# Performance work log

Hardware: AMD Instinct MI355X
Metric: run time of the kernel (lower is better)

## Reference

```python
import jax, jax.numpy as jnp
import numpy as np

B, T, S, D, H, HD, DFF, NB = 2, 2048, 2048, 768, 12, 64, 3072, 32
HID = H * HD
EPS = 1e-6
NEG = -1e9


def rmsnorm(x, w):
    # T5 RMSNorm: no mean subtraction, no bias
    var = jnp.mean(jnp.square(x), axis=-1, keepdims=True)
    return x * jax.lax.rsqrt(var + EPS) * w


def sdpa(h, kv, m, wq, wk, wv, wo):
    # h: [B,Tq,D], kv: [B,Tk,D], m: additive mask broadcastable to [B,H,Tq,Tk]
    b, tq, _ = h.shape
    tk = kv.shape[1]
    q = (h @ wq).reshape(b, tq, H, HD)
    k = (kv @ wk).reshape(b, tk, H, HD)
    v = (kv @ wv).reshape(b, tk, H, HD)
    scores = jnp.einsum('bthd,bshd->bhts', q, k) + m  # scale=1.0 (T5)
    p = jax.nn.softmax(scores, axis=-1)
    y = jnp.einsum('bhts,bshd->bthd', p, v).reshape(b, tq, HID)
    return y @ wo


def setup_inputs() -> dict:
    key = jax.random.key(0)
    ks = jax.random.split(key, 16)
    x = jax.random.normal(ks[0], (B, T, D), dtype=jnp.float32)
    # causal additive mask for decoder self-attention
    causal = jnp.tril(jnp.ones((T, T), dtype=bool))
    mask = jnp.broadcast_to(jnp.where(causal, 0.0, NEG)[None, None], (B, 1, T, T)).astype(jnp.float32)
    relative_position = jax.random.randint(ks[1], (1, 1, T, T), 0, NB)
    encoder_hidden_states = jax.random.normal(ks[2], (B, S, D), dtype=jnp.float32)
    encoder_attention_mask = jnp.zeros((B, 1, T, S), dtype=jnp.float32)
    sc = 0.02
    p = {
        'sn_w': jnp.ones((D,), jnp.float32),
        'wq': sc * jax.random.normal(ks[3], (D, HID)),
        'wk': sc * jax.random.normal(ks[4], (D, HID)),
        'wv': sc * jax.random.normal(ks[5], (D, HID)),
        'wo': sc * jax.random.normal(ks[6], (HID, D)),
        'rel_emb': sc * jax.random.normal(ks[7], (NB, H)),
        'cn_w': jnp.ones((D,), jnp.float32),
        'cwq': sc * jax.random.normal(ks[8], (D, HID)),
        'cwk': sc * jax.random.normal(ks[9], (D, HID)),
        'cwv': sc * jax.random.normal(ks[10], (D, HID)),
        'cwo': sc * jax.random.normal(ks[11], (HID, D)),
        'pn_w': jnp.ones((D,), jnp.float32),
        'ffn_wi': sc * jax.random.normal(ks[12], (D, DFF)),
        'ffn_wo': sc * jax.random.normal(ks[13], (DFF, D)),
    }
    return dict(x=x, mask=mask, relative_position=relative_position,
                encoder_hidden_states=encoder_hidden_states,
                encoder_attention_mask=encoder_attention_mask, **p)


def reference(x, mask, relative_position, encoder_hidden_states, encoder_attention_mask,
              sn_w, wq, wk, wv, wo, rel_emb, cn_w, cwq, cwk, cwv, cwo, pn_w, ffn_wi, ffn_wo):
    # self-attention with relative-position bias added into additive mask
    h = rmsnorm(x, sn_w)
    # rel_emb[relative_position]: [1,1,T,T,H] -> permute(0,1,4,2,3) -> squeeze(0) -> [1,H,T,T]
    position_bias = jnp.transpose(rel_emb[relative_position], (0, 1, 4, 2, 3))[0]
    self_mask = mask + position_bias
    y = sdpa(h, h, self_mask, wq, wk, wv, wo)
    attn_out = y + x
    # cross-attention (no relative bias -> zeros position bias)
    enc_dec_position_bias = jnp.zeros_like(encoder_attention_mask)
    h2 = rmsnorm(attn_out, cn_w)
    y2 = sdpa(h2, encoder_hidden_states, encoder_attention_mask + enc_dec_position_bias,
              cwq, cwk, cwv, cwo)
    attn_out = y2 + attn_out
    # T5 FFN: relu(x @ wi) @ wo, pre-norm, residual
    hn = rmsnorm(attn_out, pn_w)
    ff = jax.nn.relu(hn @ ffn_wi) @ ffn_wo
    return (attn_out + ff, position_bias, enc_dec_position_bias)
```

## Files before the change

kernel.cpp:

```cpp
#include <hip/hip_runtime.h>
#include <hip/hip_bf16.h>
#include <stdint.h>

#define T5_B   2
#define T5_T   2048
#define T5_S   2048
#define T5_D   768
#define T5_H   12
#define T5_HD  64
#define T5_DFF 3072
#define T5_NB  32
#define NROW   4096

typedef __attribute__((ext_vector_type(8))) short bf16x8;
typedef __attribute__((ext_vector_type(4))) short short4v;
typedef __attribute__((ext_vector_type(4))) float f32x4;

__device__ __forceinline__ unsigned short f2bf(float x) {
  unsigned int u = __float_as_uint(x);
  unsigned int r = (u + 0x7FFFu + ((u >> 16) & 1u)) >> 16;
  return (unsigned short)r;
}

__device__ __forceinline__ void load_lds16(const void* g, void* l) {
  __builtin_amdgcn_global_load_lds(
      (__attribute__((address_space(1))) void*)(const_cast<void*>(g)),
      (__attribute__((address_space(3))) void*)(l), 16, 0, 0);
}

__device__ __forceinline__ unsigned cvt_pk_bf16(float lo_, float hi_) {
  unsigned d;
  asm("v_cvt_pk_bf16_f32 %0, %1, %2" : "=v"(d) : "v"(lo_), "v"(hi_));
  return d;
}

__device__ __forceinline__ f32x4 mfma16(short4v a, short4v b, f32x4 c) {
#if __has_builtin(__builtin_amdgcn_mfma_f32_16x16x16bf16_1k)
  return __builtin_amdgcn_mfma_f32_16x16x16bf16_1k(a, b, c, 0, 0, 0);
#else
  asm volatile("v_mfma_f32_16x16x16_bf16 %0, %1, %2, %0" : "+v"(c) : "v"(a), "v"(b));
  return c;
#endif
}

struct PrepArgs {
  const float* wsrc[10];
  unsigned short* wdst[10];
  const float* enc; unsigned short* encb;
  const int* rp; unsigned char* rp8;
};

__global__ __launch_bounds__(256)
void prep_kernel(PrepArgs a) {
  __shared__ float tile[32][33];
  const int bid = blockIdx.x, tid = threadIdx.x;
  if (bid < 9216) {
    int widx, rem, Kd, Nd;
    if (bid < 4608)      { widx = bid / 576; rem = bid % 576;  Kd = 768;  Nd = 768;  }
    else if (bid < 6912) { widx = 8;         rem = bid - 4608; Kd = 768;  Nd = 3072; }
    else                 { widx = 9;         rem = bid - 6912; Kd = 3072; Nd = 768;  }
    const float* W = a.wsrc[widx];
    unsigned short* Wt = a.wdst[widx];
    int nb = Nd / 32;
    int n0 = (rem % nb) * 32, k0 = (rem / nb) * 32;
    int tx = tid & 31, ty = tid >> 5;
#pragma unroll
    for (int i = 0; i < 32; i += 8)
      tile[ty + i][tx] = W[(size_t)(k0 + ty + i) * Nd + n0 + tx];
    __syncthreads();
#pragma unroll
    for (int i = 0; i < 32; i += 8)
      Wt[(size_t)(n0 + ty + i) * Kd + k0 + tx] = f2bf(tile[tx][ty + i]);
  } else if (bid < 12288) {
    int i = (bid - 9216) * 256 + tid;
    float4 v = ((const float4*)a.enc)[i];
    unsigned long long pk = (unsigned long long)f2bf(v.x)
                          | ((unsigned long long)f2bf(v.y) << 16)
                          | ((unsigned long long)f2bf(v.z) << 32)
                          | ((unsigned long long)f2bf(v.w) << 48);
    *(unsigned long long*)(a.encb + (size_t)i * 4) = pk;
  } else {
    int idx = (bid - 12288) * 256 + tid;
    const int4* src = (const int4*)(a.rp + (size_t)idx * 16);
    int4 v0 = src[0], v1 = src[1], v2 = src[2], v3 = src[3];
    uint4 o;
    o.x = (v0.x & 31) | ((v0.y & 31) << 8) | ((v0.z & 31) << 16) | ((v0.w & 31) << 24);
    o.y = (v1.x & 31) | ((v1.y & 31) << 8) | ((v1.z & 31) << 16) | ((v1.w & 31) << 24);
    o.z = (v2.x & 31) | ((v2.y & 31) << 8) | ((v2.z & 31) << 16) | ((v2.w & 31) << 24);
    o.w = (v3.x & 31) | ((v3.y & 31) << 8) | ((v3.z & 31) << 16) | ((v3.w & 31) << 24);
    ((uint4*)a.rp8)[idx] = o;
  }
}

__global__ __launch_bounds__(256)
void rmsnorm_kernel(const float* __restrict__ in, const float* __restrict__ w,
                    unsigned short* __restrict__ out) {
  int row = blockIdx.x, tid = threadIdx.x;
  const float* r = in + (size_t)row * 768;
  float x0 = r[tid], x1 = r[tid + 256], x2 = r[tid + 512];
  float s = x0 * x0 + x1 * x1 + x2 * x2;
#pragma unroll
  for (int off = 32; off > 0; off >>= 1) s += __shfl_xor(s, off);
  __shared__ float ws_[4];
  int lane = tid & 63, wv = tid >> 6;
  if (lane == 0) ws_[wv] = s;
  __syncthreads();
  float tot = ws_[0] + ws_[1] + ws_[2] + ws_[3];
  float rinv = rsqrtf(tot * (1.0f / 768.0f) + 1e-6f);
  unsigned short* o = out + (size_t)row * 768;
  o[tid]       = f2bf(x0 * rinv * w[tid]);
  o[tid + 256] = f2bf(x1 * rinv * w[tid + 256]);
  o[tid + 512] = f2bf(x2 * rinv * w[tid + 512]);
}

__global__ __launch_bounds__(256)
void pos_bias_kernel(const int* __restrict__ rp, const float* __restrict__ rel_emb,
                     float* __restrict__ out1) {
  __shared__ float rl[384];
  int tid = threadIdx.x;
  for (int i = tid; i < 384; i += 256) rl[i] = rel_emb[i];
  __syncthreads();
  int t = blockIdx.y;
  int s = blockIdx.x * 1024 + tid * 4;
  int4 nb = *(const int4*)(rp + (size_t)t * 2048 + s);
#pragma unroll
  for (int h = 0; h < 12; ++h) {
    float4 v = make_float4(rl[nb.x * 12 + h], rl[nb.y * 12 + h],
                           rl[nb.z * 12 + h], rl[nb.w * 12 + h]);
    *(float4*)(out1 + ((size_t)h * 2048 + t) * 2048 + s) = v;
  }
}

__global__ __launch_bounds__(256)
void transpose_v_kernel(const unsigned short* __restrict__ vin, int stride,
                        unsigned short* __restrict__ vT) {
  __shared__ __align__(16) unsigned short tile[64][72];
  int t0 = blockIdx.x * 64, h = blockIdx.y, b = blockIdx.z;
  int tid = threadIdx.x;
  {
    int tl = tid >> 2, d0 = (tid & 3) * 16;
    const unsigned short* src = vin + (size_t)(b * 2048 + t0 + tl) * stride + h * 64 + d0;
    *(bf16x8*)&tile[tl][d0]     = *(const bf16x8*)src;
    *(bf16x8*)&tile[tl][d0 + 8] = *(const bf16x8*)(src + 8);
  }
  __syncthreads();
  {
    int d = tid >> 2, t1 = (tid & 3) * 16;
    unsigned short tmp[16] __attribute__((aligned(16)));
#pragma unroll
    for (int j = 0; j < 16; ++j) tmp[j] = tile[t1 + j][d];
    unsigned short* dst = vT + ((size_t)((b * 12 + h) * 64 + d)) * 2048 + t0 + t1;
    *(bf16x8*)dst       = *(bf16x8*)&tmp[0];
    *(bf16x8*)(dst + 8) = *(bf16x8*)&tmp[8];
  }
}

template <int TM, int TN, int EPI>
__global__ __launch_bounds__(256)
void gemm_bt(const unsigned short* __restrict__ A, const unsigned short* __restrict__ Bt,
             void* __restrict__ C, const float* __restrict__ res, int N, int K) {
  constexpr int WR = (TM >= 128) ? 2 : 1;
  constexpr int WC = 4 / WR;
  constexpr int AM = TM / WR / 16;
  constexpr int AN = TN / WC / 16;
  constexpr int CHA = TM / 8, CHB = TN / 8, CPW = (CHA + CHB) / 4;
  __shared__ __align__(16) unsigned short Als[TM * 64];
  __shared__ __align__(16) unsigned short Bls[TN * 64];
  const int tid = threadIdx.x, lane = tid & 63, wv = tid >> 6;
  const int lo = lane & 15, hi = lane >> 4;
  const int wr = wv / WC, wc = wv % WC;
  const int m0 = blockIdx.y * TM, n0 = blockIdx.x * TN;

  f32x4 acc[AM][AN];
#pragma unroll
  for (int i = 0; i < AM; ++i)
#pragma unroll
    for (int j = 0; j < AN; ++j) acc[i][j] = f32x4{0.f, 0.f, 0.f, 0.f};

  const int srr  = lane >> 3;
  const int scol = ((lane & 7) ^ srr) * 8;

  for (int k0 = 0; k0 < K; k0 += 64) {
    __syncthreads();
#pragma unroll
    for (int j = 0; j < CPW; ++j) {
      int c = wv * CPW + j;
      if (c < CHA)
        load_lds16(A + (size_t)(m0 + c * 8 + srr) * K + k0 + scol, Als + c * 512);
      else {
        int c2 = c - CHA;
        load_lds16(Bt + (size_t)(n0 + c2 * 8 + srr) * K + k0 + scol, Bls + c2 * 512);
      }
    }
    __syncthreads();
#pragma unroll
    for (int kk = 0; kk < 2; ++kk) {
      bf16x8 af[AM], bfr[AN];
#pragma unroll
      for (int i = 0; i < AM; ++i) {
        int row = wr * (AM * 16) + i * 16 + lo;
        unsigned by = (unsigned)(row * 128) + ((unsigned)(((kk * 4 + hi) ^ (row & 7))) << 4);
        af[i] = *(const bf16x8*)((const char*)Als + by);
      }
#pragma unroll
      for (int j = 0; j < AN; ++j) {
        int row = wc * (AN * 16) + j * 16 + lo;
        unsigned by = (unsigned)(row * 128) + ((unsigned)(((kk * 4 + hi) ^ (row & 7))) << 4);
        bfr[j] = *(const bf16x8*)((const char*)Bls + by);
      }
      __builtin_amdgcn_s_setprio(1);
#pragma unroll
      for (int i = 0; i < AM; ++i)
#pragma unroll
        for (int j = 0; j < AN; ++j)
          acc[i][j] = __builtin_amdgcn_mfma_f32_16x16x32_bf16(af[i], bfr[j], acc[i][j], 0, 0, 0);
      __builtin_amdgcn_s_setprio(0);
    }
  }

#pragma unroll
  for (int mi = 0; mi < AM; ++mi)
#pragma unroll
    for (int ni = 0; ni < AN; ++ni) {
      int row = m0 + wr * (AM * 16) + mi * 16 + hi * 4;
      int col = n0 + wc * (AN * 16) + ni * 16 + lo;
#pragma unroll
      for (int r = 0; r < 4; ++r) {
        float v = acc[mi][ni][r];
        size_t idx = (size_t)(row + r) * N + col;
        if (EPI == 0) {
          ((unsigned short*)C)[idx] = f2bf(v);
        } else if (EPI == 1) {
          ((float*)C)[idx] = v + res[idx];
        } else {
          ((unsigned short*)C)[idx] = f2bf(fmaxf(v, 0.0f));
        }
      }
    }
}

template <bool SELF>
__global__ __launch_bounds__(256)
void attn_kernel(const unsigned short* __restrict__ qp, int qstride,
                 const unsigned short* __restrict__ kp, int kstride,
                 const unsigned short* __restrict__ vT,
                 const unsigned char* __restrict__ rp8, const float* __restrict__ rel_emb,
                 unsigned short* __restrict__ yp) {
  __shared__ __align__(16) unsigned short Kls[2][64 * 64];
  __shared__ __align__(16) unsigned short Vls[2][64 * 64];
  __shared__ __align__(16) unsigned char rp8t[SELF ? 2 * 4096 : 16];
  __shared__ float rel_l[32];

  const int tid = threadIdx.x, lane = tid & 63, wv = tid >> 6;
  const int lo = lane & 15, hi = lane >> 4;
  const int q0 = blockIdx.x * 64, h = blockIdx.y, b = blockIdx.z;

  if (SELF && tid < 32) rel_l[tid] = rel_emb[tid * 12 + h];

  const int q = q0 + wv * 16 + lo;
  const unsigned short* qr = qp + (size_t)(b * T5_T + q) * qstride + h * 64 + hi * 8;
  const bf16x8 qf0 = *(const bf16x8*)qr;
  const bf16x8 qf1 = *(const bf16x8*)(qr + 32);

  f32x4 Oacc[4];
#pragma unroll
  for (int i = 0; i < 4; ++i) Oacc[i] = f32x4{0.f, 0.f, 0.f, 0.f};
  float m_ = -3.0e38f, l_ = 0.f;

  const int ntiles = SELF ? (blockIdx.x + 1) : (T5_S / 64);

  const int krr = lane >> 3;
  const int kd0 = ((lane & 7) ^ krr) * 8;

  auto stage = [&](int kt, int bsel) {
    const int s0 = kt * 64;
#pragma unroll
    for (int j = 0; j < 2; ++j) {
      int c = wv * 2 + j;
      int rr = c * 8 + krr;
      load_lds16(kp + (size_t)(b * 2048 + s0 + rr) * kstride + h * 64 + kd0, &Kls[bsel][c * 512]);
      load_lds16(vT + (size_t)((b * 12 + h) * 64 + rr) * 2048 + s0 + kd0,    &Vls[bsel][c * 512]);
    }
    if (SELF)
      load_lds16(rp8 + (size_t)(q0 + wv * 16 + (lane >> 2)) * 2048 + s0 + (lane & 3) * 16,
                 &rp8t[bsel * 4096 + wv * 1024]);
  };

  stage(0, 0);

  for (int kt = 0; kt < ntiles; ++kt) {
    const int bsel = kt & 1;
    const int s0 = kt * 64;
    asm volatile("s_waitcnt vmcnt(0)" ::: "memory");
    __syncthreads();
    if (kt + 1 < ntiles) stage(kt + 1, bsel ^ 1);

    const unsigned short* Kb = &Kls[bsel][0];
    const unsigned short* Vb = &Vls[bsel][0];

    f32x4 S[4];
    __builtin_amdgcn_s_setprio(1);
#pragma unroll
    for (int ct = 0; ct < 4; ++ct) {
      int krow = ct * 16 + lo;
      unsigned by0 = ((unsigned)(krow * 128 + hi * 16))      ^ ((unsigned)(krow & 7) << 4);
      unsigned by1 = ((unsigned)(krow * 128 + 64 + hi * 16)) ^ ((unsigned)(krow & 7) << 4);
      bf16x8 kf0 = *(const bf16x8*)((const char*)Kb + by0);
      bf16x8 kf1 = *(const bf16x8*)((const char*)Kb + by1);
      f32x4 sa = f32x4{0.f, 0.f, 0.f, 0.f};
      sa = __builtin_amdgcn_mfma_f32_16x16x32_bf16(kf0, qf0, sa, 0, 0, 0);
      sa = __builtin_amdgcn_mfma_f32_16x16x32_bf16(kf1, qf1, sa, 0, 0, 0);
      S[ct] = sa;
    }
    __builtin_amdgcn_s_setprio(0);

    if (SELF) {
      const bool edge = (kt == ntiles - 1);
      const unsigned char* rt = &rp8t[bsel * 4096 + wv * 1024];
#pragma unroll
      for (int ct = 0; ct < 4; ++ct) {
        unsigned nb4 = *(const unsigned*)&rt[lo * 64 + ct * 16 + hi * 4];
#pragma unroll
        for (int r = 0; r < 4; ++r) {
          int s = s0 + ct * 16 + hi * 4 + r;
          float sc = S[ct][r] + rel_l[(nb4 >> (8 * r)) & 31u];
          if (edge && s > q) sc = -1e30f;
          S[ct][r] = sc;
        }
      }
    }

    float tm = S[0][0];
#pragma unroll
    for (int ct = 0; ct < 4; ++ct)
#pragma unroll
      for (int r = 0; r < 4; ++r) tm = fmaxf(tm, S[ct][r]);
    tm = fmaxf(tm, __shfl_xor(tm, 16));
    tm = fmaxf(tm, __shfl_xor(tm, 32));
    float mn = fmaxf(m_, tm);
    float alpha = __expf(m_ - mn);
    float rs = 0.f;
#pragma unroll
    for (int ct = 0; ct < 4; ++ct)
#pragma unroll
      for (int r = 0; r < 4; ++r) { float e = __expf(S[ct][r] - mn); S[ct][r] = e; rs += e; }
    rs += __shfl_xor(rs, 16);
    rs += __shfl_xor(rs, 32);
    l_ = l_ * alpha + rs;
    m_ = mn;
#pragma unroll
    for (int dt = 0; dt < 4; ++dt)
#pragma unroll
      for (int r = 0; r < 4; ++r) Oacc[dt][r] *= alpha;

    short4v pf[4];
#pragma unroll
    for (int ct = 0; ct < 4; ++ct) {
      union { unsigned u[2]; short4v s; } cv;
      cv.u[0] = cvt_pk_bf16(S[ct][0], S[ct][1]);
      cv.u[1] = cvt_pk_bf16(S[ct][2], S[ct][3]);
      pf[ct] = cv.s;
    }

    __builtin_amdgcn_s_setprio(1);
#pragma unroll
    for (int dt = 0; dt < 4; ++dt) {
      int vrow = dt * 16 + lo;
#pragma unroll
      for (int ct = 0; ct < 4; ++ct) {
        unsigned vb = ((unsigned)(vrow * 128 + ct * 32 + hi * 8)) ^ ((unsigned)(vrow & 7) << 4);
        short4v vf = *(const short4v*)((const char*)Vb + vb);
        Oacc[dt] = mfma16(vf, pf[ct], Oacc[dt]);
      }
    }
    __builtin_amdgcn_s_setprio(0);
  }

#if !__has_builtin(__builtin_amdgcn_mfma_f32_16x16x16bf16_1k)
  asm volatile("s_nop 7\n\ts_nop 7" ::: );
#endif

  float inv = 1.0f / l_;
  unsigned short* yr = yp + (size_t)(b * T5_T + q) * 768 + h * 64 + hi * 4;
#pragma unroll
  for (int dt = 0; dt < 4; ++dt) {
    unsigned long long pk = (unsigned long long)f2bf(Oacc[dt][0] * inv)
                          | ((unsigned long long)f2bf(Oacc[dt][1] * inv) << 16)
                          | ((unsigned long long)f2bf(Oacc[dt][2] * inv) << 32)
                          | ((unsigned long long)f2bf(Oacc[dt][3] * inv) << 48);
    *(unsigned long long*)(yr + dt * 16) = pk;
  }
}

extern "C" void kernel_launch(void* const* d_in, const int* in_sizes, int n_in,
                              void* d_out, int out_size, void* d_ws, size_t ws_size,
                              hipStream_t stream) {
  (void)in_sizes; (void)n_in; (void)out_size; (void)ws_size;
  const float* x    = (const float*)d_in[0];
  const int*   rp   = (const int*)d_in[2];
  const float* enc  = (const float*)d_in[3];
  const float* sn_w = (const float*)d_in[5];
  const float* wq   = (const float*)d_in[6];
  const float* wk   = (const float*)d_in[7];
  const float* wvw  = (const float*)d_in[8];
  const float* wo   = (const float*)d_in[9];
  const float* rel  = (const float*)d_in[10];
  const float* cn_w = (const float*)d_in[11];
  const float* cwq  = (const float*)d_in[12];
  const float* cwk  = (const float*)d_in[13];
  const float* cwv  = (const float*)d_in[14];
  const float* cwo  = (const float*)d_in[15];
  const float* pn_w = (const float*)d_in[16];
  const float* wi   = (const float*)d_in[17];
  const float* wo2  = (const float*)d_in[18];

  float* out0 = (float*)d_out;
  float* out1 = out0 + (size_t)NROW * T5_D;
  float* out2 = out1 + (size_t)T5_H * T5_T * T5_T;

  char* ws = (char*)d_ws;
  size_t off = 0;
  auto alloc = [&](size_t bytes) { char* p = ws + off; off += (bytes + 255) & ~(size_t)255; return p; };
  unsigned short* wqkvT = (unsigned short*)alloc((size_t)2304 * 768 * 2);
  unsigned short* woT   = (unsigned short*)alloc((size_t)768 * 768 * 2);
  unsigned short* wckvT = (unsigned short*)alloc((size_t)1536 * 768 * 2);
  unsigned short* wcqT  = (unsigned short*)alloc((size_t)768 * 768 * 2);
  unsigned short* wcoT  = (unsigned short*)alloc((size_t)768 * 768 * 2);
  unsigned short* wiT   = (unsigned short*)alloc((size_t)3072 * 768 * 2);
  unsigned short* woT2  = (unsigned short*)alloc((size_t)768 * 3072 * 2);
  unsigned short* normb = (unsigned short*)alloc((size_t)NROW * 768 * 2);
  unsigned short* encb  = (unsigned short*)alloc((size_t)NROW * 768 * 2);
  unsigned short* ybuf  = (unsigned short*)alloc((size_t)NROW * 768 * 2);
  float*          attn  = (float*)alloc((size_t)NROW * 768 * 4);
  unsigned char*  rp8p  = (unsigned char*)alloc((size_t)2048 * 2048);
  unsigned short* big   = (unsigned short*)alloc((size_t)NROW * 3072 * 2);
  unsigned short* vT    = big + (size_t)NROW * 2304;

  dim3 blk(256);

  {
    PrepArgs pa;
    pa.wsrc[0] = wq;  pa.wdst[0] = wqkvT;
    pa.wsrc[1] = wk;  pa.wdst[1] = wqkvT + 768 * 768;
    pa.wsrc[2] = wvw; pa.wdst[2] = wqkvT + 2 * 768 * 768;
    pa.wsrc[3] = wo;  pa.wdst[3] = woT;
    pa.wsrc[4] = cwk; pa.wdst[4] = wckvT;
    pa.wsrc[5] = cwv; pa.wdst[5] = wckvT + 768 * 768;
    pa.wsrc[6] = cwq; pa.wdst[6] = wcqT;
    pa.wsrc[7] = cwo; pa.wdst[7] = wcoT;
    pa.wsrc[8] = wi;  pa.wdst[8] = wiT;
    pa.wsrc[9] = wo2; pa.wdst[9] = woT2;
    pa.enc = enc; pa.encb = encb; pa.rp = rp; pa.rp8 = rp8p;
    prep_kernel<<<13312, blk, 0, stream>>>(pa);
  }

  rmsnorm_kernel<<<NROW, blk, 0, stream>>>(x, sn_w, normb);

  gemm_bt<128, 128, 0><<<dim3(18, 32), blk, 0, stream>>>(normb, wqkvT, big, nullptr, 2304, 768);
  transpose_v_kernel<<<dim3(32, 12, 2), blk, 0, stream>>>(big + 1536, 2304, vT);
  attn_kernel<true><<<dim3(32, 12, 2), blk, 0, stream>>>(big, 2304, big + 768, 2304, vT, rp8p, rel, ybuf);
  gemm_bt<64, 128, 1><<<dim3(6, 64), blk, 0, stream>>>(ybuf, woT, attn, x, 768, 768);

  pos_bias_kernel<<<dim3(2, 2048), blk, 0, stream>>>(rp, rel, out1);
  hipMemsetAsync(out2, 0, (size_t)T5_B * T5_T * T5_S * 4, stream);

  rmsnorm_kernel<<<NROW, blk, 0, stream>>>(attn, cn_w, normb);
  gemm_bt<128, 128, 0><<<dim3(12, 32), blk, 0, stream>>>(encb, wckvT, big + (size_t)NROW * 768, nullptr, 1536, 768);
  gemm_bt<64, 128, 0><<<dim3(6, 64), blk, 0, stream>>>(normb, wcqT, big, nullptr, 768, 768);
  transpose_v_kernel<<<dim3(32, 12, 2), blk, 0, stream>>>(big + (size_t)NROW * 768 + 768, 1536, vT);
  attn_kernel<false><<<dim3(32, 12, 2), blk, 0, stream>>>(big, 768, big + (size_t)NROW * 768, 1536, vT,
                                                          nullptr, nullptr, ybuf);
  gemm_bt<64, 128, 1><<<dim3(6, 64), blk, 0, stream>>>(ybuf, wcoT, attn, attn, 768, 768);

  rmsnorm_kernel<<<NROW, blk, 0, stream>>>(attn, pn_w, normb);
  gemm_bt<128, 128, 2><<<dim3(24, 32), blk, 0, stream>>>(normb, wiT, big, nullptr, 3072, 768);
  gemm_bt<64, 128, 1><<<dim3(6, 64), blk, 0, stream>>>(big, woT2, out0, attn, 768, 3072);
}
```

Before: 398.6 us.

## Double-buffer GEMM, XCD-remap tiles, pair causal query tiles, fuse zero fill

The GEMM gets double-buffered LDS with a prefetch of the next K tile and raw barriers, plus an XCD-aware remap of workgroup index to tile so that neighbouring tiles share an L2. The attention kernel now handles two query tiles per block: for causal self-attention it pairs tile i with tile 31-i to balance the triangle work, and for cross-attention it takes two adjacent tiles so each K/V load serves both. The zeroing of out2 moves from hipMemsetAsync into pos_bias_kernel. The costs are doubled LDS and more registers, which can reduce occupancy, and half as many attention blocks.

```diff
diff --git a/kernel.cpp b/kernel.cpp
--- a/kernel.cpp
+++ b/kernel.cpp
@@ -115,7 +115,7 @@
 
 __global__ __launch_bounds__(256)
 void pos_bias_kernel(const int* __restrict__ rp, const float* __restrict__ rel_emb,
-                     float* __restrict__ out1) {
+                     float* __restrict__ out1, float* __restrict__ out2) {
   __shared__ float rl[384];
   int tid = threadIdx.x;
   for (int i = tid; i < 384; i += 256) rl[i] = rel_emb[i];
@@ -129,6 +129,10 @@
                            rl[nb.z * 12 + h], rl[nb.w * 12 + h]);
     *(float4*)(out1 + ((size_t)h * 2048 + t) * 2048 + s) = v;
   }
+  size_t base = (((size_t)blockIdx.y * 2 + blockIdx.x) * 256 + tid) * 8;
+  float4 z = make_float4(0.f, 0.f, 0.f, 0.f);
+  *(float4*)(out2 + base)     = z;
+  *(float4*)(out2 + base + 4) = z;
 }
 
 __global__ __launch_bounds__(256)
@@ -164,12 +168,18 @@
   constexpr int AM = TM / WR / 16;
   constexpr int AN = TN / WC / 16;
   constexpr int CHA = TM / 8, CHB = TN / 8, CPW = (CHA + CHB) / 4;
-  __shared__ __align__(16) unsigned short Als[TM * 64];
-  __shared__ __align__(16) unsigned short Bls[TN * 64];
+  __shared__ __align__(16) unsigned short Als[2][TM * 64];
+  __shared__ __align__(16) unsigned short Bls[2][TN * 64];
   const int tid = threadIdx.x, lane = tid & 63, wv = tid >> 6;
   const int lo = lane & 15, hi = lane >> 4;
   const int wr = wv / WC, wc = wv % WC;
-  const int m0 = blockIdx.y * TM, n0 = blockIdx.x * TN;
+
+  int gx = gridDim.x;
+  int nwg = gx * gridDim.y;
+  int f = blockIdx.y * gx + blockIdx.x;
+  int q8 = nwg >> 3, r8 = nwg & 7, xcd = f & 7, base = f >> 3;
+  int wg = (xcd < r8 ? xcd * (q8 + 1) : r8 * (q8 + 1) + (xcd - r8) * q8) + base;
+  const int m0 = (wg / gx) * TM, n0 = (wg % gx) * TN;
 
   f32x4 acc[AM][AN];
 #pragma unroll
@@ -180,19 +190,31 @@
   const int srr  = lane >> 3;
   const int scol = ((lane & 7) ^ srr) * 8;
 
-  for (int k0 = 0; k0 < K; k0 += 64) {
-    __syncthreads();
+  auto stage = [&](int k0, int bsel) {
 #pragma unroll
     for (int j = 0; j < CPW; ++j) {
       int c = wv * CPW + j;
       if (c < CHA)
-        load_lds16(A + (size_t)(m0 + c * 8 + srr) * K + k0 + scol, Als + c * 512);
+        load_lds16(A + (size_t)(m0 + c * 8 + srr) * K + k0 + scol, &Als[bsel][c * 512]);
       else {
         int c2 = c - CHA;
-        load_lds16(Bt + (size_t)(n0 + c2 * 8 + srr) * K + k0 + scol, Bls + c2 * 512);
+        load_lds16(Bt + (size_t)(n0 + c2 * 8 + srr) * K + k0 + scol, &Bls[bsel][c2 * 512]);
       }
     }
-    __syncthreads();
+  };
+
+  stage(0, 0);
+  const int nIt = K >> 6;
+  for (int it = 0; it < nIt; ++it) {
+    const int bsel = it & 1;
+    if (it + 1 < nIt) {
+      stage((it + 1) << 6, bsel ^ 1);
+      asm volatile("s_waitcnt vmcnt(%0)" :: "n"(CPW) : "memory");
+    } else {
+      asm volatile("s_waitcnt vmcnt(0)" ::: "memory");
+    }
+    __builtin_amdgcn_s_barrier();
+    __builtin_amdgcn_sched_barrier(0);
 #pragma unroll
     for (int kk = 0; kk < 2; ++kk) {
       bf16x8 af[AM], bfr[AN];
@@ -200,13 +222,13 @@
       for (int i = 0; i < AM; ++i) {
         int row = wr * (AM * 16) + i * 16 + lo;
         unsigned by = (unsigned)(row * 128) + ((unsigned)(((kk * 4 + hi) ^ (row & 7))) << 4);
-        af[i] = *(const bf16x8*)((const char*)Als + by);
+        af[i] = *(const bf16x8*)((const char*)&Als[bsel][0] + by);
       }
 #pragma unroll
       for (int j = 0; j < AN; ++j) {
         int row = wc * (AN * 16) + j * 16 + lo;
         unsigned by = (unsigned)(row * 128) + ((unsigned)(((kk * 4 + hi) ^ (row & 7))) << 4);
-        bfr[j] = *(const bf16x8*)((const char*)Bls + by);
+        bfr[j] = *(const bf16x8*)((const char*)&Bls[bsel][0] + by);
       }
       __builtin_amdgcn_s_setprio(1);
 #pragma unroll
@@ -216,6 +238,8 @@
           acc[i][j] = __builtin_amdgcn_mfma_f32_16x16x32_bf16(af[i], bfr[j], acc[i][j], 0, 0, 0);
       __builtin_amdgcn_s_setprio(0);
     }
+    __builtin_amdgcn_sched_barrier(0);
+    __builtin_amdgcn_s_barrier();
   }
 
 #pragma unroll
@@ -246,28 +270,33 @@
                  const unsigned short* __restrict__ vT,
                  const unsigned char* __restrict__ rp8, const float* __restrict__ rel_emb,
                  unsigned short* __restrict__ yp) {
-  __shared__ __align__(16) unsigned short Kls[2][64 * 64];
-  __shared__ __align__(16) unsigned short Vls[2][64 * 64];
-  __shared__ __align__(16) unsigned char rp8t[SELF ? 2 * 4096 : 16];
+  __shared__ __align__(16) unsigned short Kls[2][4096];
+  __shared__ __align__(16) unsigned short Vls[2][4096];
+  __shared__ __align__(16) unsigned char rp8t[SELF ? 2 * 8192 : 16];
   __shared__ float rel_l[32];
 
   const int tid = threadIdx.x, lane = tid & 63, wv = tid >> 6;
   const int lo = lane & 15, hi = lane >> 4;
-  const int q0 = blockIdx.x * 64, h = blockIdx.y, b = blockIdx.z;
+  const int h = blockIdx.y, b = blockIdx.z;
+  const int qta = SELF ? (int)blockIdx.x : (int)blockIdx.x * 2;
+  const int qtb = SELF ? 31 - (int)blockIdx.x : (int)blockIdx.x * 2 + 1;
+  const int ntiles = SELF ? qtb + 1 : 32;
 
   if (SELF && tid < 32) rel_l[tid] = rel_emb[tid * 12 + h];
 
-  const int q = q0 + wv * 16 + lo;
-  const unsigned short* qr = qp + (size_t)(b * T5_T + q) * qstride + h * 64 + hi * 8;
-  const bf16x8 qf0 = *(const bf16x8*)qr;
-  const bf16x8 qf1 = *(const bf16x8*)(qr + 32);
-
-  f32x4 Oacc[4];
-#pragma unroll
-  for (int i = 0; i < 4; ++i) Oacc[i] = f32x4{0.f, 0.f, 0.f, 0.f};
-  float m_ = -3.0e38f, l_ = 0.f;
-
-  const int ntiles = SELF ? (blockIdx.x + 1) : (T5_S / 64);
+  const int qA = qta * 64 + wv * 16 + lo;
+  const int qB = qtb * 64 + wv * 16 + lo;
+  const unsigned short* qrA = qp + (size_t)(b * T5_T + qA) * qstride + h * 64 + hi * 8;
+  const unsigned short* qrB = qp + (size_t)(b * T5_T + qB) * qstride + h * 64 + hi * 8;
+  const bf16x8 qa0 = *(const bf16x8*)qrA;
+  const bf16x8 qa1 = *(const bf16x8*)(qrA + 32);
+  const bf16x8 qb0 = *(const bf16x8*)qrB;
+  const bf16x8 qb1 = *(const bf16x8*)(qrB + 32);
+
+  f32x4 OA[4], OB[4];
+  float mA = -3.0e38f, lA = 0.f, mB = -3.0e38f, lB = 0.f;
+#pragma unroll
+  for (int i = 0; i < 4; ++i) { OA[i] = f32x4{0.f, 0.f, 0.f, 0.f}; OB[i] = f32x4{0.f, 0.f, 0.f, 0.f}; }
 
   const int krr = lane >> 3;
   const int kd0 = ((lane & 7) ^ krr) * 8;
@@ -281,23 +310,18 @@
       load_lds16(kp + (size_t)(b * 2048 + s0 + rr) * kstride + h * 64 + kd0, &Kls[bsel][c * 512]);
       load_lds16(vT + (size_t)((b * 12 + h) * 64 + rr) * 2048 + s0 + kd0,    &Vls[bsel][c * 512]);
     }
-    if (SELF)
-      load_lds16(rp8 + (size_t)(q0 + wv * 16 + (lane >> 2)) * 2048 + s0 + (lane & 3) * 16,
-                 &rp8t[bsel * 4096 + wv * 1024]);
+    if (SELF) {
+      load_lds16(rp8 + (size_t)(qtb * 64 + wv * 16 + (lane >> 2)) * 2048 + s0 + (lane & 3) * 16,
+                 &rp8t[bsel * 8192 + 4096 + wv * 1024]);
+      if (kt <= qta)
+        load_lds16(rp8 + (size_t)(qta * 64 + wv * 16 + (lane >> 2)) * 2048 + s0 + (lane & 3) * 16,
+                   &rp8t[bsel * 8192 + wv * 1024]);
+    }
   };
 
-  stage(0, 0);
-
-  for (int kt = 0; kt < ntiles; ++kt) {
-    const int bsel = kt & 1;
-    const int s0 = kt * 64;
-    asm volatile("s_waitcnt vmcnt(0)" ::: "memory");
-    __syncthreads();
-    if (kt + 1 < ntiles) stage(kt + 1, bsel ^ 1);
-
-    const unsigned short* Kb = &Kls[bsel][0];
-    const unsigned short* Vb = &Vls[bsel][0];
-
+  auto qcomp = [&](const bf16x8& qf0, const bf16x8& qf1, f32x4* Oc, float& m_, float& l_,
+                   const unsigned char* rt, int qrow, bool edge, int s0,
+                   const unsigned short* Kb, const unsigned short* Vb) {
     f32x4 S[4];
     __builtin_amdgcn_s_setprio(1);
 #pragma unroll
@@ -315,8 +339,6 @@
     __builtin_amdgcn_s_setprio(0);
 
     if (SELF) {
-      const bool edge = (kt == ntiles - 1);
-      const unsigned char* rt = &rp8t[bsel * 4096 + wv * 1024];
 #pragma unroll
       for (int ct = 0; ct < 4; ++ct) {
         unsigned nb4 = *(const unsigned*)&rt[lo * 64 + ct * 16 + hi * 4];
@@ -324,7 +346,7 @@
         for (int r = 0; r < 4; ++r) {
           int s = s0 + ct * 16 + hi * 4 + r;
           float sc = S[ct][r] + rel_l[(nb4 >> (8 * r)) & 31u];
-          if (edge && s > q) sc = -1e30f;
+          if (edge && s > qrow) sc = -1e30f;
           S[ct][r] = sc;
         }
       }
@@ -351,7 +373,7 @@
 #pragma unroll
     for (int dt = 0; dt < 4; ++dt)
 #pragma unroll
-      for (int r = 0; r < 4; ++r) Oacc[dt][r] *= alpha;
+      for (int r = 0; r < 4; ++r) Oc[dt][r] *= alpha;
 
     short4v pf[4];
 #pragma unroll
@@ -370,25 +392,58 @@
       for (int ct = 0; ct < 4; ++ct) {
         unsigned vb = ((unsigned)(vrow * 128 + ct * 32 + hi * 8)) ^ ((unsigned)(vrow & 7) << 4);
         short4v vf = *(const short4v*)((const char*)Vb + vb);
-        Oacc[dt] = mfma16(vf, pf[ct], Oacc[dt]);
+        Oc[dt] = mfma16(vf, pf[ct], Oc[dt]);
       }
     }
     __builtin_amdgcn_s_setprio(0);
+  };
+
+  stage(0, 0);
+
+  for (int kt = 0; kt < ntiles; ++kt) {
+    const int bsel = kt & 1;
+    const int s0 = kt * 64;
+    asm volatile("s_waitcnt vmcnt(0)" ::: "memory");
+    __syncthreads();
+    if (kt + 1 < ntiles) stage(kt + 1, bsel ^ 1);
+
+    const unsigned short* Kb = &Kls[bsel][0];
+    const unsigned short* Vb = &Vls[bsel][0];
+
+    if (!SELF || kt <= qta)
+      qcomp(qa0, qa1, OA, mA, lA, &rp8t[bsel * 8192 + wv * 1024], qA,
+            SELF && kt == qta, s0, Kb, Vb);
+    qcomp(qb0, qb1, OB, mB, lB, &rp8t[bsel * 8192 + 4096 + wv * 1024], qB,
+          SELF && kt == qtb, s0, Kb, Vb);
   }
 
 #if !__has_builtin(__builtin_amdgcn_mfma_f32_16x16x16bf16_1k)
   asm volatile("s_nop 7\n\ts_nop 7" ::: );
 #endif
 
-  float inv = 1.0f / l_;
-  unsigned short* yr = yp + (size_t)(b * T5_T + q) * 768 + h * 64 + hi * 4;
-#pragma unroll
-  for (int dt = 0; dt < 4; ++dt) {
-    unsigned long long pk = (unsigned long long)f2bf(Oacc[dt][0] * inv)
-                          | ((unsigned long long)f2bf(Oacc[dt][1] * inv) << 16)
-                          | ((unsigned long long)f2bf(Oacc[dt][2] * inv) << 32)
-                          | ((unsigned long long)f2bf(Oacc[dt][3] * inv) << 48);
-    *(unsigned long long*)(yr + dt * 16) = pk;
+  {
+    float inv = 1.0f / lA;
+    unsigned short* yr = yp + (size_t)(b * T5_T + qA) * 768 + h * 64 + hi * 4;
+#pragma unroll
+    for (int dt = 0; dt < 4; ++dt) {
+      unsigned long long pk = (unsigned long long)f2bf(OA[dt][0] * inv)
+                            | ((unsigned long long)f2bf(OA[dt][1] * inv) << 16)
+                            | ((unsigned long long)f2bf(OA[dt][2] * inv) << 32)
+                            | ((unsigned long long)f2bf(OA[dt][3] * inv) << 48);
+      *(unsigned long long*)(yr + dt * 16) = pk;
+    }
+  }
+  {
+    float inv = 1.0f / lB;
+    unsigned short* yr = yp + (size_t)(b * T5_T + qB) * 768 + h * 64 + hi * 4;
+#pragma unroll
+    for (int dt = 0; dt < 4; ++dt) {
+      unsigned long long pk = (unsigned long long)f2bf(OB[dt][0] * inv)
+                            | ((unsigned long long)f2bf(OB[dt][1] * inv) << 16)
+                            | ((unsigned long long)f2bf(OB[dt][2] * inv) << 32)
+                            | ((unsigned long long)f2bf(OB[dt][3] * inv) << 48);
+      *(unsigned long long*)(yr + dt * 16) = pk;
+    }
   }
 }
 
@@ -458,17 +513,16 @@
 
   gemm_bt<128, 128, 0><<<dim3(18, 32), blk, 0, stream>>>(normb, wqkvT, big, nullptr, 2304, 768);
   transpose_v_kernel<<<dim3(32, 12, 2), blk, 0, stream>>>(big + 1536, 2304, vT);
-  attn_kernel<true><<<dim3(32, 12, 2), blk, 0, stream>>>(big, 2304, big + 768, 2304, vT, rp8p, rel, ybuf);
+  attn_kernel<true><<<dim3(16, 12, 2), blk, 0, stream>>>(big, 2304, big + 768, 2304, vT, rp8p, rel, ybuf);
   gemm_bt<64, 128, 1><<<dim3(6, 64), blk, 0, stream>>>(ybuf, woT, attn, x, 768, 768);
 
-  pos_bias_kernel<<<dim3(2, 2048), blk, 0, stream>>>(rp, rel, out1);
-  hipMemsetAsync(out2, 0, (size_t)T5_B * T5_T * T5_S * 4, stream);
+  pos_bias_kernel<<<dim3(2, 2048), blk, 0, stream>>>(rp, rel, out1, out2);
 
   rmsnorm_kernel<<<NROW, blk, 0, stream>>>(attn, cn_w, normb);
   gemm_bt<128, 128, 0><<<dim3(12, 32), blk, 0, stream>>>(encb, wckvT, big + (size_t)NROW * 768, nullptr, 1536, 768);
   gemm_bt<64, 128, 0><<<dim3(6, 64), blk, 0, stream>>>(normb, wcqT, big, nullptr, 768, 768);
   transpose_v_kernel<<<dim3(32, 12, 2), blk, 0, stream>>>(big + (size_t)NROW * 768 + 768, 1536, vT);
-  attn_kernel<false><<<dim3(32, 12, 2), blk, 0, stream>>>(big, 768, big + (size_t)NROW * 768, 1536, vT,
+  attn_kernel<false><<<dim3(16, 12, 2), blk, 0, stream>>>(big, 768, big + (size_t)NROW * 768, 1536, vT,
                                                           nullptr, nullptr, ybuf);
   gemm_bt<64, 128, 1><<<dim3(6, 64), blk, 0, stream>>>(ybuf, wcoT, attn, attn, 768, 768);
 
```

Result: faster. 386.9 us (-2.9%).
